# Kernel tuning notes

Measured on AMD Instinct MI355X. Metric: run time of the kernel, lower is better.

## Reference

```python
import jax, jax.numpy as jnp
import numpy as np

EPS = 1e-06
N_HEADS = 16


def elu_feature_map(x):
    return jax.nn.elu(x) + 1.0


def setup_inputs() -> dict:
    key = jax.random.key(0)
    ks = jax.random.split(key, 5)
    B, S, D = 4, 4096, 1024
    scale = 1.0 / np.sqrt(D)
    x = jax.random.normal(ks[0], (B, S, D), dtype=jnp.float32)
    Wq = jax.random.normal(ks[1], (D, D), dtype=jnp.float32) * scale
    Wk = jax.random.normal(ks[2], (D, D), dtype=jnp.float32) * scale
    Wv = jax.random.normal(ks[3], (D, D), dtype=jnp.float32) * scale
    Wo = jax.random.normal(ks[4], (D, D), dtype=jnp.float32) * scale
    return {"x": x, "Wq": Wq, "Wk": Wk, "Wv": Wv, "Wo": Wo}


def reference(x, Wq, Wk, Wv, Wo):
    B, S, D = x.shape
    H = N_HEADS
    hd = D // H
    # nn.Linear(bias=False): y = x @ W.T
    q = (x @ Wq.T).reshape(B, S, H, hd)
    k = (x @ Wk.T).reshape(B, S, H, hd)
    v = (x @ Wv.T).reshape(B, S, H, hd)
    q = elu_feature_map(q)
    k = elu_feature_map(k)
    KV = jnp.einsum('bshd,bshe->bhde', k, v)          # [B,H,hd,hd]
    out = jnp.einsum('bshd,bhde->bshe', q, KV)        # [B,S,H,hd]
    k_sum = k.sum(axis=1)                             # [B,H,hd]
    z = jnp.einsum('bshd,bhd->bsh', q, k_sum)[..., None]
    out = out / (z + EPS)
    out = out.reshape(B, S, D)
    return out @ Wo.T
```

## Files before the change

### kernel.cpp

```cpp
#include <hip/hip_runtime.h>
#include <hip/hip_bf16.h>

#define BB 4
#define SS 4096
#define DD 1024
#define HH 16
#define HD 64
#define MM (BB * SS)
#define KK DD
#define NN DD

typedef __bf16 bf16x8 __attribute__((ext_vector_type(8)));
typedef float f32x4 __attribute__((ext_vector_type(4)));

typedef __attribute__((address_space(3))) void lds_void_t;
typedef const __attribute__((address_space(1))) void glb_void_t;

__global__ __launch_bounds__(256)
void cvt_f32_bf16(const float* __restrict__ in, __hip_bfloat16* __restrict__ out, int n4) {
    int i = blockIdx.x * 256 + threadIdx.x;
    if (i >= n4) return;
    float4 v = ((const float4*)in)[i];
    union { __hip_bfloat16 h[4]; uint2 u; } r;
    r.h[0] = __float2bfloat16(v.x);
    r.h[1] = __float2bfloat16(v.y);
    r.h[2] = __float2bfloat16(v.z);
    r.h[3] = __float2bfloat16(v.w);
    ((uint2*)out)[i] = r.u;
}

#define RD_A(dst, idx)                                                                   \
    dst[0] = *(const bf16x8*)(sAb + ((idx) * 16 + lr) * 128 + ((lq * 16) ^ swz));        \
    dst[1] = *(const bf16x8*)(sAb + ((idx) * 16 + lr) * 128 + (((64) + lq * 16) ^ swz));

#define MFMA2(i0, i1, va, vb)                                                                         \
    __builtin_amdgcn_s_setprio(1);                                                                    \
    _Pragma("unroll")                                                                                 \
    for (int j = 0; j < 4; ++j) {                                                                     \
        acc[i0][j] = __builtin_amdgcn_mfma_f32_16x16x32_bf16(va[0], bfr[j][0], acc[i0][j], 0, 0, 0);  \
        acc[i0][j] = __builtin_amdgcn_mfma_f32_16x16x32_bf16(va[1], bfr[j][1], acc[i0][j], 0, 0, 0);  \
        acc[i1][j] = __builtin_amdgcn_mfma_f32_16x16x32_bf16(vb[0], bfr[j][0], acc[i1][j], 0, 0, 0);  \
        acc[i1][j] = __builtin_amdgcn_mfma_f32_16x16x32_bf16(vb[1], bfr[j][1], acc[i1][j], 0, 0, 0);  \
    }                                                                                                 \
    __builtin_amdgcn_s_setprio(0);

template<int MODE>
__global__ __launch_bounds__(512, 2)
void gemm256(const __hip_bfloat16* __restrict__ Ain,
             const __hip_bfloat16* __restrict__ Bin,
             __hip_bfloat16* __restrict__ Obf,
             float* __restrict__ Of32)
{
    __shared__ __align__(16) __hip_bfloat16 sA[2][2][128 * 64];
    __shared__ __align__(16) __hip_bfloat16 sB[2][2][128 * 64];

    const int bid = blockIdx.x;
    const int mt  = ((bid & 7) << 3) | ((bid >> 3) & 7);
    const int nt  = bid >> 6;
    const int m0  = mt << 8;
    const int n0  = nt << 8;

    const int t      = threadIdx.x;
    const int lane   = t & 63;
    const int w      = t >> 6;
    const int warp_m = w >> 2;
    const int warp_n = w & 3;
    const int halfB  = warp_n >> 1;
    const int bn     = (warp_n & 1) << 6;
    const int lr     = lane & 15;
    const int lq     = lane >> 4;
    const int swz    = (lr & 7) << 4;

    const int trow = t >> 3;
    const int tcb  = (((t & 7) ^ ((t >> 3) & 7)) << 4);

    auto stage = [&](int ht) {
        if (ht >= 64) return;
        const int ts   = ht >> 2;
        const int kind = ht & 3;
        const int half = kind & 1;
        #pragma unroll
        for (int i = 0; i < 2; ++i) {
            const int row = i * 64 + trow;
            if (kind >= 2) {
                __builtin_amdgcn_global_load_lds(
                    (glb_void_t*)(Ain + (size_t)(m0 + half * 128 + row) * 1024 + ts * 64 + (tcb >> 1)),
                    (lds_void_t*)(&sA[ts & 1][half][(i * 512 + t) * 8]), 16, 0, 0);
            } else {
                __builtin_amdgcn_global_load_lds(
                    (glb_void_t*)(Bin + (size_t)(n0 + half * 128 + row) * 1024 + ts * 64 + (tcb >> 1)),
                    (lds_void_t*)(&sB[ts & 1][half][(i * 512 + t) * 8]), 16, 0, 0);
            }
        }
    };

    f32x4 acc[8][4];
    #pragma unroll
    for (int i = 0; i < 8; ++i)
        #pragma unroll
        for (int j = 0; j < 4; ++j)
            acc[i][j] = (f32x4){0.f, 0.f, 0.f, 0.f};

    stage(0); stage(1); stage(2); stage(3);
    stage(4); stage(5); stage(6);
    asm volatile("s_waitcnt vmcnt(6)" ::: "memory");
    __builtin_amdgcn_s_barrier();

    #pragma unroll 2
    for (int kt = 0; kt < 16; ++kt) {
        const char* sAb = (const char*)&sA[kt & 1][warp_m][0];
        const char* sBb = (const char*)&sB[kt & 1][halfB][0];
        bf16x8 bfr[4][2];
        bf16x8 a0[2], a1[2], a2[2], a3[2], a4[2], a5[2], a6[2], a7[2];

        #pragma unroll
        for (int j = 0; j < 4; ++j) {
            bfr[j][0] = *(const bf16x8*)(sBb + (bn + j * 16 + lr) * 128 + ((lq * 16) ^ swz));
            bfr[j][1] = *(const bf16x8*)(sBb + (bn + j * 16 + lr) * 128 + ((64 + lq * 16) ^ swz));
        }
        __builtin_amdgcn_sched_barrier(0);
        RD_A(a0, 0); RD_A(a1, 1);
        __builtin_amdgcn_sched_barrier(0);
        RD_A(a2, 2); RD_A(a3, 3);
        __builtin_amdgcn_sched_barrier(0);
        stage(4 * kt + 7);

        asm volatile("s_waitcnt lgkmcnt(4)" ::: "memory");
        __builtin_amdgcn_sched_barrier(0);
        MFMA2(0, 1, a0, a1);
        __builtin_amdgcn_sched_barrier(0);
        RD_A(a4, 4); RD_A(a5, 5);
        __builtin_amdgcn_sched_barrier(0);
        RD_A(a6, 6); RD_A(a7, 7);

        asm volatile("s_waitcnt lgkmcnt(8)" ::: "memory");
        __builtin_amdgcn_sched_barrier(0);
        MFMA2(2, 3, a2, a3);
        __builtin_amdgcn_s_barrier();
        stage(4 * kt + 8);
        stage(4 * kt + 9);

        asm volatile("s_waitcnt lgkmcnt(4)" ::: "memory");
        __builtin_amdgcn_sched_barrier(0);
        MFMA2(4, 5, a4, a5);
        asm volatile("s_waitcnt lgkmcnt(0)" ::: "memory");
        __builtin_amdgcn_sched_barrier(0);
        MFMA2(6, 7, a6, a7);
        __builtin_amdgcn_s_barrier();
        stage(4 * kt + 10);

        if (kt < 14)       { asm volatile("s_waitcnt vmcnt(6)" ::: "memory"); }
        else if (kt == 14) { asm volatile("s_waitcnt vmcnt(0)" ::: "memory"); }
        __builtin_amdgcn_s_barrier();
    }

    if constexpr (MODE == 0) {
        const int wsel = n0 >> 10;
        const int nb   = n0 & 1023;
        __hip_bfloat16* Op = Obf + (size_t)wsel * ((size_t)MM * KK);
        const bool doelu = (wsel < 2);
        #pragma unroll
        for (int i = 0; i < 8; ++i)
            #pragma unroll
            for (int j = 0; j < 4; ++j)
                #pragma unroll
                for (int r = 0; r < 4; ++r) {
                    const int row = m0 + warp_m * 128 + i * 16 + lq * 4 + r;
                    const int col = nb + warp_n * 64 + j * 16 + lr;
                    float v = acc[i][j][r];
                    if (doelu) v = (v > 0.f) ? v + 1.f : __expf(v);
                    Op[(size_t)row * 1024 + col] = __float2bfloat16(v);
                }
    } else {
        #pragma unroll
        for (int i = 0; i < 8; ++i)
            #pragma unroll
            for (int j = 0; j < 4; ++j)
                #pragma unroll
                for (int r = 0; r < 4; ++r) {
                    const int row = m0 + warp_m * 128 + i * 16 + lq * 4 + r;
                    const int col = n0 + warp_n * 64 + j * 16 + lr;
                    Of32[(size_t)row * 1024 + col] = acc[i][j][r];
                }
    }
}

#define KV_SPLIT 8
__global__ __launch_bounds__(256)
void kv_mfma(const __hip_bfloat16* __restrict__ Kt,
             const __hip_bfloat16* __restrict__ Vt,
             float* __restrict__ KVp)
{
    __shared__ __hip_bfloat16 sK[128 * 64];
    __shared__ __hip_bfloat16 sV[128 * 64];
    __shared__ float sRed[65 * 66];

    const int bh = blockIdx.x;
    const int b  = bh >> 4;
    const int h  = bh & 15;
    const int sp = blockIdx.y;
    const int t  = threadIdx.x;
    const int lane = t & 63;
    const int wv = t >> 6;
    const int lr = lane & 15;
    const int lq = lane >> 4;
    const int s0blk = sp * (SS / KV_SPLIT);

    const __hip_bfloat16* kbase = Kt + ((size_t)b * SS + s0blk) * DD + h * HD;
    const __hip_bfloat16* vbase = Vt + ((size_t)b * SS + s0blk) * DD + h * HD;

    f32x4 acc[4][4];
    f32x4 ksacc[4];
    #pragma unroll
    for (int i = 0; i < 4; i++) {
        ksacc[i] = (f32x4){0.f, 0.f, 0.f, 0.f};
        #pragma unroll
        for (int j = 0; j < 4; j++)
            acc[i][j] = (f32x4){0.f, 0.f, 0.f, 0.f};
    }

    bf16x8 ones;
    #pragma unroll
    for (int j = 0; j < 8; j++) ones[j] = (__bf16)1.0f;

    for (int sc = 0; sc < 4; sc++) {
        const int srow0 = sc * 128;
        #pragma unroll
        for (int i = 0; i < 4; i++) {
            int slot = i * 256 + t;
            int r = slot >> 3;
            int o = (t & 7) ^ ((r >> 3) & 3);
            size_t goff = (size_t)(srow0 + r) * DD + o * 8;
            __builtin_amdgcn_global_load_lds(
                (glb_void_t*)(kbase + goff),
                (lds_void_t*)((char*)sK + slot * 16), 16, 0, 0);
            __builtin_amdgcn_global_load_lds(
                (glb_void_t*)(vbase + goff),
                (lds_void_t*)((char*)sV + slot * 16), 16, 0, 0);
        }
        __syncthreads();

        bf16x8 ak[4], bv[4];
        #pragma unroll
        for (int i = 0; i < 4; i++) {
            #pragma unroll
            for (int j = 0; j < 8; j++) {
                int r = wv * 32 + lq * 8 + j;
                int d = i * 16 + lr;
                int idx = r * 64 + (((d >> 3) ^ lq) << 3) + (d & 7);
                ak[i][j] = ((const __bf16*)sK)[idx];
                bv[i][j] = ((const __bf16*)sV)[idx];
            }
        }
        #pragma unroll
        for (int i = 0; i < 4; i++) {
            #pragma unroll
            for (int j = 0; j < 4; j++)
                acc[i][j] = __builtin_amdgcn_mfma_f32_16x16x32_bf16(ak[i], bv[j], acc[i][j], 0, 0, 0);
            ksacc[i] = __builtin_amdgcn_mfma_f32_16x16x32_bf16(ak[i], ones, ksacc[i], 0, 0, 0);
        }
        __syncthreads();
    }

    for (int w = 0; w < 4; w++) {
        if (wv == w) {
            #pragma unroll
            for (int i = 0; i < 4; i++) {
                #pragma unroll
                for (int j = 0; j < 4; j++) {
                    float* p = &sRed[(j * 16 + lr) * 66 + i * 16 + lq * 4];
                    if (w == 0) {
                        #pragma unroll
                        for (int r = 0; r < 4; r++) p[r] = acc[i][j][r];
                    } else {
                        #pragma unroll
                        for (int r = 0; r < 4; r++) p[r] += acc[i][j][r];
                    }
                }
                if (lr == 0) {
                    float* p = &sRed[64 * 66 + i * 16 + lq * 4];
                    if (w == 0) {
                        #pragma unroll
                        for (int r = 0; r < 4; r++) p[r] = ksacc[i][r];
                    } else {
                        #pragma unroll
                        for (int r = 0; r < 4; r++) p[r] += ksacc[i][r];
                    }
                }
            }
        }
        __syncthreads();
    }

    float* outp = KVp + (size_t)(sp * 64 + bh) * (65 * 64);
    #pragma unroll
    for (int i = 0; i < 17; i++) {
        int idx = i * 256 + t;
        if (idx < 65 * 64) {
            int e = idx >> 6, d = idx & 63;
            outp[idx] = sRed[e * 66 + d];
        }
    }
}

__global__ __launch_bounds__(256)
void kv_reduce(const float* __restrict__ KVp,
               __hip_bfloat16* __restrict__ KVt,
               float* __restrict__ KS)
{
    const int bh = blockIdx.x;
    const int t  = threadIdx.x;
    #pragma unroll
    for (int i = 0; i < 16; i++) {
        int idx = i * 256 + t;
        float s = 0.f;
        #pragma unroll
        for (int sp = 0; sp < KV_SPLIT; sp++)
            s += KVp[((size_t)(sp * 64 + bh) * 65) * 64 + idx];
        KVt[(size_t)bh * 4096 + idx] = __float2bfloat16(s);
    }
    if (t < 64) {
        float s = 0.f;
        #pragma unroll
        for (int sp = 0; sp < KV_SPLIT; sp++)
            s += KVp[((size_t)(sp * 64 + bh) * 65 + 64) * 64 + t];
        KS[bh * 64 + t] = s;
    }
}

__global__ __launch_bounds__(256)
void attn_mfma(const __hip_bfloat16* __restrict__ Q,
               const __hip_bfloat16* __restrict__ KVt,
               const float* __restrict__ KS,
               __hip_bfloat16* __restrict__ O)
{
    const int bh = blockIdx.x;
    const int b  = bh >> 4;
    const int h  = bh & 15;
    const int s0 = blockIdx.y * 128;
    const int t  = threadIdx.x;
    const int lane = t & 63;
    const int wv = t >> 6;

    __shared__ __align__(16) __hip_bfloat16 sQ[128][72];
    __shared__ __align__(16) __hip_bfloat16 sKVt[64][72];
    __shared__ float sKS[64];
    __shared__ float sZ[128];

    {
        const float4* kvp = (const float4*)(KVt + (size_t)bh * 4096);
        #pragma unroll
        for (int i = 0; i < 2; i++) {
            int c = i * 256 + t;
            *(float4*)(&sKVt[c >> 3][(c & 7) * 8]) = kvp[c];
        }
        if (t < 64) sKS[t] = KS[bh * 64 + t];
    }
    {
        const __hip_bfloat16* qp = Q + ((size_t)b * SS + s0) * DD + h * HD;
        int r  = t >> 1;
        int c0 = (t & 1) * 32;
        #pragma unroll
        for (int i = 0; i < 32; i += 8)
            *(float4*)(&sQ[r][c0 + i]) = *(const float4*)(qp + (size_t)r * DD + c0 + i);
    }
    __syncthreads();

    if (t < 128) {
        float z = 0.f;
        #pragma unroll
        for (int d8 = 0; d8 < 64; d8 += 8) {
            bf16x8 qv = *(const bf16x8*)(&sQ[t][d8]);
            #pragma unroll
            for (int j = 0; j < 8; j++) z += (float)qv[j] * sKS[d8 + j];
        }
        sZ[t] = 1.f / (z + 1e-6f);
    }

    const int lr = lane & 15;
    const int lq = lane >> 4;
    f32x4 acc[2][4];
    #pragma unroll
    for (int i = 0; i < 2; i++)
        #pragma unroll
        for (int j = 0; j < 4; j++)
            acc[i][j] = (f32x4){0.f, 0.f, 0.f, 0.f};

    bf16x8 af[2][2], bfv[4][2];
    #pragma unroll
    for (int ks = 0; ks < 2; ks++) {
        #pragma unroll
        for (int i = 0; i < 2; i++)
            af[i][ks] = *(const bf16x8*)(&sQ[wv * 32 + i * 16 + lr][lq * 8 + ks * 32]);
        #pragma unroll
        for (int j = 0; j < 4; j++)
            bfv[j][ks] = *(const bf16x8*)(&sKVt[j * 16 + lr][lq * 8 + ks * 32]);
    }
    #pragma unroll
    for (int i = 0; i < 2; i++)
        #pragma unroll
        for (int j = 0; j < 4; j++) {
            acc[i][j] = __builtin_amdgcn_mfma_f32_16x16x32_bf16(af[i][0], bfv[j][0], acc[i][j], 0, 0, 0);
            acc[i][j] = __builtin_amdgcn_mfma_f32_16x16x32_bf16(af[i][1], bfv[j][1], acc[i][j], 0, 0, 0);
        }
    __syncthreads();

    __hip_bfloat16* op = O + ((size_t)b * SS + s0) * DD + h * HD;
    #pragma unroll
    for (int i = 0; i < 2; i++)
        #pragma unroll
        for (int j = 0; j < 4; j++)
            #pragma unroll
            for (int r = 0; r < 4; r++) {
                int row = wv * 32 + i * 16 + lq * 4 + r;
                int col = j * 16 + lr;
                op[(size_t)row * DD + col] = __float2bfloat16(acc[i][j][r] * sZ[row]);
            }
}

extern "C" void kernel_launch(void* const* d_in, const int* in_sizes, int n_in,
                              void* d_out, int out_size, void* d_ws, size_t ws_size,
                              hipStream_t stream) {
    const float* x  = (const float*)d_in[0];
    const float* Wq = (const float*)d_in[1];
    const float* Wk = (const float*)d_in[2];
    const float* Wv = (const float*)d_in[3];
    const float* Wo = (const float*)d_in[4];
    float* out = (float*)d_out;

    char* ws = (char*)d_ws;
    const size_t XB_BYTES = (size_t)MM * KK * 2;
    const size_t WB_BYTES = (size_t)NN * KK * 2;
    __hip_bfloat16* xb  = (__hip_bfloat16*)(ws);
    __hip_bfloat16* wqb = (__hip_bfloat16*)(ws + XB_BYTES);
    __hip_bfloat16* wkb = (__hip_bfloat16*)(ws + XB_BYTES + WB_BYTES);
    __hip_bfloat16* wvb = (__hip_bfloat16*)(ws + XB_BYTES + 2 * WB_BYTES);
    __hip_bfloat16* wob = (__hip_bfloat16*)(ws + XB_BYTES + 3 * WB_BYTES);
    __hip_bfloat16* qb  = (__hip_bfloat16*)(ws + XB_BYTES + 4 * WB_BYTES);
    __hip_bfloat16* kb  = (__hip_bfloat16*)(ws + 2 * XB_BYTES + 4 * WB_BYTES);
    __hip_bfloat16* vb  = (__hip_bfloat16*)(ws + 3 * XB_BYTES + 4 * WB_BYTES);
    __hip_bfloat16* KVt = (__hip_bfloat16*)(ws + 4 * XB_BYTES + 4 * WB_BYTES);
    float*          KS  = (float*)(ws + 4 * XB_BYTES + 4 * WB_BYTES + 524288);
    float* KVp = (float*)(ws);
    __hip_bfloat16* ab = xb;

    const int XN = MM * KK;
    const int WN = NN * KK;

    cvt_f32_bf16<<<XN / 4 / 256, 256, 0, stream>>>(x,  xb,  XN / 4);
    cvt_f32_bf16<<<WN / 4 / 256, 256, 0, stream>>>(Wq, wqb, WN / 4);
    cvt_f32_bf16<<<WN / 4 / 256, 256, 0, stream>>>(Wk, wkb, WN / 4);
    cvt_f32_bf16<<<WN / 4 / 256, 256, 0, stream>>>(Wv, wvb, WN / 4);
    cvt_f32_bf16<<<WN / 4 / 256, 256, 0, stream>>>(Wo, wob, WN / 4);

    gemm256<0><<<768, 512, 0, stream>>>(xb, wqb, qb, nullptr);

    kv_mfma<<<dim3(BB * HH, KV_SPLIT), 256, 0, stream>>>(kb, vb, KVp);
    kv_reduce<<<BB * HH, 256, 0, stream>>>(KVp, KVt, KS);

    attn_mfma<<<dim3(BB * HH, SS / 128), 256, 0, stream>>>(qb, KVt, KS, ab);

    gemm256<1><<<256, 512, 0, stream>>>(ab, wob, nullptr, out);
}
```

Baseline: 336.6 us.

## Write K/V transposed per head from QKV GEMM and drop LDS staging in KV kernel

The QKV GEMM epilogue now stores K and V in a per-(batch, head, dim) transposed layout with sequence contiguous, packing four bf16 values per store. The KV outer-product kernel can then load MFMA operands straight from global memory as 16-byte vectors, with no LDS staging and no per-element swizzled LDS gathers or barriers. The trade is that the GEMM epilogue stores become strided in the transposed layout, which may hurt write coalescing.

```diff
diff --git a/kernel.cpp b/kernel.cpp
--- a/kernel.cpp
+++ b/kernel.cpp
@@ -158,19 +158,39 @@
         const int wsel = n0 >> 10;
         const int nb   = n0 & 1023;
         __hip_bfloat16* Op = Obf + (size_t)wsel * ((size_t)MM * KK);
-        const bool doelu = (wsel < 2);
-        #pragma unroll
-        for (int i = 0; i < 8; ++i)
-            #pragma unroll
-            for (int j = 0; j < 4; ++j)
+        if (wsel == 0) {
+            #pragma unroll
+            for (int i = 0; i < 8; ++i)
                 #pragma unroll
-                for (int r = 0; r < 4; ++r) {
-                    const int row = m0 + warp_m * 128 + i * 16 + lq * 4 + r;
-                    const int col = nb + warp_n * 64 + j * 16 + lr;
-                    float v = acc[i][j][r];
-                    if (doelu) v = (v > 0.f) ? v + 1.f : __expf(v);
-                    Op[(size_t)row * 1024 + col] = __float2bfloat16(v);
+                for (int j = 0; j < 4; ++j)
+                    #pragma unroll
+                    for (int r = 0; r < 4; ++r) {
+                        const int row = m0 + warp_m * 128 + i * 16 + lq * 4 + r;
+                        const int col = nb + warp_n * 64 + j * 16 + lr;
+                        float v = acc[i][j][r];
+                        v = (v > 0.f) ? v + 1.f : __expf(v);
+                        Op[(size_t)row * 1024 + col] = __float2bfloat16(v);
+                    }
+        } else {
+            const bool doelu = (wsel == 1);
+            #pragma unroll
+            for (int i = 0; i < 8; ++i)
+                #pragma unroll
+                for (int j = 0; j < 4; ++j) {
+                    const int row0 = m0 + warp_m * 128 + i * 16 + lq * 4;
+                    const int col  = nb + warp_n * 64 + j * 16 + lr;
+                    const int b    = row0 >> 12;
+                    const int s    = row0 & 4095;
+                    union { __hip_bfloat16 hh[4]; uint2 u; } pk;
+                    #pragma unroll
+                    for (int r = 0; r < 4; ++r) {
+                        float v = acc[i][j][r];
+                        if (doelu) v = (v > 0.f) ? v + 1.f : __expf(v);
+                        pk.hh[r] = __float2bfloat16(v);
+                    }
+                    *(uint2*)(Op + ((size_t)((b * 16 + (col >> 6)) * 64 + (col & 63)) * 4096 + s)) = pk.u;
                 }
+        }
     } else {
         #pragma unroll
         for (int i = 0; i < 8; ++i)
@@ -187,27 +207,23 @@
 
 #define KV_SPLIT 8
 __global__ __launch_bounds__(256)
-void kv_mfma(const __hip_bfloat16* __restrict__ Kt,
-             const __hip_bfloat16* __restrict__ Vt,
+void kv_gemm(const __hip_bfloat16* __restrict__ KB,
+             const __hip_bfloat16* __restrict__ VB,
              float* __restrict__ KVp)
 {
-    __shared__ __hip_bfloat16 sK[128 * 64];
-    __shared__ __hip_bfloat16 sV[128 * 64];
     __shared__ float sRed[65 * 66];
 
     const int bh = blockIdx.x;
-    const int b  = bh >> 4;
-    const int h  = bh & 15;
     const int sp = blockIdx.y;
     const int t  = threadIdx.x;
     const int lane = t & 63;
     const int wv = t >> 6;
     const int lr = lane & 15;
     const int lq = lane >> 4;
-    const int s0blk = sp * (SS / KV_SPLIT);
-
-    const __hip_bfloat16* kbase = Kt + ((size_t)b * SS + s0blk) * DD + h * HD;
-    const __hip_bfloat16* vbase = Vt + ((size_t)b * SS + s0blk) * DD + h * HD;
+
+    const __hip_bfloat16* kbase = KB + (size_t)bh * 64 * 4096;
+    const __hip_bfloat16* vbase = VB + (size_t)bh * 64 * 4096;
+    const int k0w = sp * 512 + wv * 128 + lq * 8;
 
     f32x4 acc[4][4];
     f32x4 ksacc[4];
@@ -223,43 +239,22 @@
     #pragma unroll
     for (int j = 0; j < 8; j++) ones[j] = (__bf16)1.0f;
 
-    for (int sc = 0; sc < 4; sc++) {
-        const int srow0 = sc * 128;
-        #pragma unroll
-        for (int i = 0; i < 4; i++) {
-            int slot = i * 256 + t;
-            int r = slot >> 3;
-            int o = (t & 7) ^ ((r >> 3) & 3);
-            size_t goff = (size_t)(srow0 + r) * DD + o * 8;
-            __builtin_amdgcn_global_load_lds(
-                (glb_void_t*)(kbase + goff),
-                (lds_void_t*)((char*)sK + slot * 16), 16, 0, 0);
-            __builtin_amdgcn_global_load_lds(
-                (glb_void_t*)(vbase + goff),
-                (lds_void_t*)((char*)sV + slot * 16), 16, 0, 0);
-        }
-        __syncthreads();
-
+    #pragma unroll
+    for (int c = 0; c < 4; ++c) {
+        const int k0 = k0w + c * 32;
         bf16x8 ak[4], bv[4];
         #pragma unroll
-        for (int i = 0; i < 4; i++) {
-            #pragma unroll
-            for (int j = 0; j < 8; j++) {
-                int r = wv * 32 + lq * 8 + j;
-                int d = i * 16 + lr;
-                int idx = r * 64 + (((d >> 3) ^ lq) << 3) + (d & 7);
-                ak[i][j] = ((const __bf16*)sK)[idx];
-                bv[i][j] = ((const __bf16*)sV)[idx];
-            }
-        }
-        #pragma unroll
-        for (int i = 0; i < 4; i++) {
-            #pragma unroll
-            for (int j = 0; j < 4; j++)
+        for (int i = 0; i < 4; ++i) {
+            ak[i] = *(const bf16x8*)(kbase + (size_t)(i * 16 + lr) * 4096 + k0);
+            bv[i] = *(const bf16x8*)(vbase + (size_t)(i * 16 + lr) * 4096 + k0);
+        }
+        #pragma unroll
+        for (int i = 0; i < 4; ++i) {
+            #pragma unroll
+            for (int j = 0; j < 4; ++j)
                 acc[i][j] = __builtin_amdgcn_mfma_f32_16x16x32_bf16(ak[i], bv[j], acc[i][j], 0, 0, 0);
             ksacc[i] = __builtin_amdgcn_mfma_f32_16x16x32_bf16(ak[i], ones, ksacc[i], 0, 0, 0);
         }
-        __syncthreads();
     }
 
     for (int w = 0; w < 4; w++) {
@@ -455,7 +450,7 @@
 
     gemm256<0><<<768, 512, 0, stream>>>(xb, wqb, qb, nullptr);
 
-    kv_mfma<<<dim3(BB * HH, KV_SPLIT), 256, 0, stream>>>(kb, vb, KVp);
+    kv_gemm<<<dim3(BB * HH, KV_SPLIT), 256, 0, stream>>>(kb, vb, KVp);
     kv_reduce<<<BB * HH, 256, 0, stream>>>(KVp, KVt, KS);
 
     attn_mfma<<<dim3(BB * HH, SS / 128), 256, 0, stream>>>(qb, KVt, KS, ab);
```

After: 336.1 us. Within noise of the previous version (-0.2%).
